# Kernel tuning notes

Measured on AMD Instinct MI355X. Metric: run time of the kernel, lower is better.

The kernel has to match this reference:

```python
import jax, jax.numpy as jnp
import numpy as np

SIGMA = 300.0      # args.sigma (temporal gaussian kernel width, frames)
DECAY = 0.9        # args.memory_decay; avg() uses weight = 1/decay per older entry
W_TIME = 1.0       # args.temporal_weight
ORIG_LOSS = 1.0    # args.originalloss_weight
EPS = 1e-7         # BCE clamp


def _get_msg(bank_values, bank_times, bank_mask, ids, times, future):
    """Vectorized MessagePassing.get_msg: per-(id,time) gather of stored
    messages, temporal-kernel + decay weighted average. Mirrors avg():
    out = sum_i dw_i * kernel_i * v_i / sum_i dw_i, dw_i = (1/decay)^rank_i
    with rank over entries passing the past/future condition, zeros if empty."""
    vals = bank_values[ids]                      # [N, M, C]
    ts = bank_times[ids].astype(jnp.float32)     # [N, M]
    mk = bank_mask[ids]                          # [N, M]
    t0 = times.astype(jnp.float32)[:, None]      # [N, 1]
    cond = (ts > t0) if future else (ts < t0)
    m = (mk & cond).astype(vals.dtype)           # [N, M]
    kern = jnp.exp(-((ts - t0) ** 2) / (2.0 * SIGMA ** 2))
    rank = jnp.cumsum(m, axis=1) - m             # exclusive rank among valid entries
    dw = ((1.0 / DECAY) ** rank) * m             # decay weights, masked
    num = jnp.einsum('nm,nmc->nc', dw * kern, vals)
    den = jnp.sum(dw, axis=1, keepdims=True)     # denominator excludes kernel (as avg())
    msg = jnp.where(den > 0, num / jnp.maximum(den, EPS), 0.0)
    return msg * W_TIME


def _bce(p, t):
    p = jnp.clip(p, EPS, 1.0 - EPS)
    return -jnp.mean(t * jnp.log(p) + (1.0 - t) * jnp.log(1.0 - p))


def setup_inputs() -> dict:
    key = jax.random.key(0)
    k = jax.random.split(key, 8)
    N, C, NUM_IDS, M = 512, 157, 10000, 20
    return {
        'a': jax.random.normal(k[0], (N, C), jnp.float32),
        'aa': jax.random.normal(k[1], (N, C, C), jnp.float32),
        'target': jax.random.uniform(k[2], (N, C), jnp.float32),
        'bank_values': jax.random.uniform(k[3], (NUM_IDS, M, C), jnp.float32),
        'bank_times': jax.random.randint(k[4], (NUM_IDS, M), 0, 1000, jnp.int32),
        'bank_mask': jnp.ones((NUM_IDS, M), dtype=bool),
        'ids': jax.random.randint(k[5], (N,), 0, NUM_IDS, jnp.int32),
        'times': jax.random.randint(k[6], (N,), 0, 1000, jnp.int32),
    }


def reference(a, aa, target, bank_values, bank_times, bank_mask, ids, times):
    # msg/fmsg come from stored (detached) data in the original
    msg = jax.lax.stop_gradient(_get_msg(bank_values, bank_times, bank_mask, ids, times, future=False))
    fmsg = jax.lax.stop_gradient(_get_msg(bank_values, bank_times, bank_mask, ids, times, future=True))
    # qa = a + sum_i aa[n,i,j]*msg[n,i] + sum_j aa[n,i,j]*fmsg[n,j]
    qa = a + jnp.einsum('nij,ni->nj', aa, msg) + jnp.einsum('nij,nj->ni', aa, fmsg)
    qa = jax.nn.sigmoid(qa)
    loss = _bce(qa, target) + _bce(jax.nn.sigmoid(a), target) * ORIG_LOSS
    # training, adjustment=False: pastloss = futureloss = 0
    loss = loss / 3.0
    return qa, loss
```

## Files before the change

### kernel.cpp

```cpp
#include <hip/hip_runtime.h>
#include <math.h>

#define N 512
#define C 157
#define M 20

__device__ __forceinline__ float sigmoidf_(float x) {
    return 1.0f / (1.0f + __expf(-x));
}

__global__ __launch_bounds__(256) void atf_main_kernel(
    const float* __restrict__ a,
    const float* __restrict__ aa,
    const float* __restrict__ target,
    const float* __restrict__ bank_values,
    const int* __restrict__ bank_times,
    const int* __restrict__ bank_mask,
    const int* __restrict__ ids,
    const int* __restrict__ times,
    float* __restrict__ out,
    double* __restrict__ loss_acc)
{
    const int n    = blockIdx.x;
    const int tid  = threadIdx.x;
    const int wave = tid >> 6;
    const int lane = tid & 63;

    __shared__ float s_ts[M];
    __shared__ int   s_mk[M];
    __shared__ float s_msg[C];
    __shared__ float s_fmsg[C];
    __shared__ float s_row[C];
    __shared__ float s_colp[4][C];
    __shared__ float s_red[4];

    const int   id = ids[n];
    const float t0 = (float)times[n];

    if (tid < M) {
        s_ts[tid] = (float)bank_times[(size_t)id * M + tid];
        s_mk[tid] = (bank_mask[(size_t)id * M + tid] != 0) ? 1 : 0;
    }
    __syncthreads();

    if (tid < C) {
        const float inv2s2 = 1.0f / (2.0f * 300.0f * 300.0f);
        const float INVDEC = 1.0f / 0.9f;
        float accP = 0.f, accF = 0.f, denP = 0.f, denF = 0.f;
        float wP = 1.f, wF = 1.f;
        const float* vb = bank_values + (size_t)id * M * C + tid;
        #pragma unroll
        for (int m = 0; m < M; ++m) {
            const float ts = s_ts[m];
            const float d  = ts - t0;
            const float kern = __expf(-d * d * inv2s2);
            const float v = vb[m * C];
            const bool mk = (s_mk[m] != 0);
            if (mk && ts < t0) { accP += wP * kern * v; denP += wP; wP *= INVDEC; }
            if (mk && ts > t0) { accF += wF * kern * v; denF += wF; wF *= INVDEC; }
        }
        s_msg[tid]  = (denP > 0.f) ? accP / fmaxf(denP, 1e-7f) : 0.0f;
        s_fmsg[tid] = (denF > 0.f) ? accF / fmaxf(denF, 1e-7f) : 0.0f;
    }
    __syncthreads();

    const float* aan = aa + (size_t)n * C * C;
    const int j0 = lane, j1 = lane + 64, j2 = lane + 128;
    float col0 = 0.f, col1 = 0.f, col2 = 0.f;
    const float f0 = s_fmsg[j0];
    const float f1 = (j1 < C) ? s_fmsg[j1] : 0.0f;
    const float f2 = (j2 < C) ? s_fmsg[j2] : 0.0f;

    for (int i = wave; i < C; i += 4) {
        const float* row = aan + i * C;
        const float mi = s_msg[i];
        const float v0 = row[j0];
        const float v1 = (j1 < C) ? row[j1] : 0.0f;
        const float v2 = (j2 < C) ? row[j2] : 0.0f;
        col0 += v0 * mi;
        col1 += v1 * mi;
        col2 += v2 * mi;
        float rp = v0 * f0 + v1 * f1 + v2 * f2;
        #pragma unroll
        for (int off = 32; off > 0; off >>= 1) rp += __shfl_down(rp, off, 64);
        if (lane == 0) s_row[i] = rp;
    }
    s_colp[wave][j0] = col0;
    if (j1 < C) s_colp[wave][j1] = col1;
    if (j2 < C) s_colp[wave][j2] = col2;
    __syncthreads();

    float local = 0.0f;
    if (tid < C) {
        const float colsum = s_colp[0][tid] + s_colp[1][tid] + s_colp[2][tid] + s_colp[3][tid];
        const float av = a[(size_t)n * C + tid];
        const float qlin = av + colsum + s_row[tid];
        const float p = sigmoidf_(qlin);
        out[(size_t)n * C + tid] = p;

        const float t = target[(size_t)n * C + tid];
        float pc = fminf(fmaxf(p, 1e-7f), 1.0f - 1e-7f);
        float pa = sigmoidf_(av);
        pa = fminf(fmaxf(pa, 1e-7f), 1.0f - 1e-7f);
        local = t * logf(pc) + (1.0f - t) * logf(1.0f - pc)
              + t * logf(pa) + (1.0f - t) * logf(1.0f - pa);
    }
    #pragma unroll
    for (int off = 32; off > 0; off >>= 1) local += __shfl_down(local, off, 64);
    if (lane == 0) s_red[wave] = local;
    __syncthreads();
    if (tid == 0) {
        const double s = (double)(s_red[0] + s_red[1] + s_red[2] + s_red[3]);
        atomicAdd(loss_acc, s);
    }
}

__global__ void atf_finalize_kernel(const double* __restrict__ loss_acc,
                                    float* __restrict__ out)
{
    out[N * C] = (float)(-(*loss_acc) / ((double)(N * C) * 3.0));
}

extern "C" void kernel_launch(void* const* d_in, const int* in_sizes, int n_in,
                              void* d_out, int out_size, void* d_ws, size_t ws_size,
                              hipStream_t stream) {
    const float* a           = (const float*)d_in[0];
    const float* aa          = (const float*)d_in[1];
    const float* target      = (const float*)d_in[2];
    const float* bank_values = (const float*)d_in[3];
    const int*   bank_times  = (const int*)d_in[4];
    const int*   bank_mask   = (const int*)d_in[5];
    const int*   ids         = (const int*)d_in[6];
    const int*   times       = (const int*)d_in[7];

    float*  out      = (float*)d_out;
    double* loss_acc = (double*)d_ws;

    hipMemsetAsync(d_ws, 0, sizeof(double), stream);
    atf_main_kernel<<<N, 256, 0, stream>>>(a, aa, target, bank_values, bank_times,
                                           bank_mask, ids, times, out, loss_acc);
    atf_finalize_kernel<<<1, 1, 0, stream>>>(loss_acc, out);
}
```

Baseline: 229.7 us.

## Unroll aa row loop by two with nontemporal loads; replace atomic loss with partials

The aa streaming loop now handles two rows per wave per iteration, which puts more independent loads in flight and interleaves two shuffle reductions. The loads use nontemporal hints because aa is read only once. The double atomicAdd and the memset are replaced by per-block float partials that a 256-thread finalize kernel reduces. This removes one launch and the atomic contention, but adds register pressure and a slightly different summation order.

```diff
diff --git a/kernel.cpp b/kernel.cpp
--- a/kernel.cpp
+++ b/kernel.cpp
@@ -7,6 +7,9 @@
 
 __device__ __forceinline__ float sigmoidf_(float x) {
     return 1.0f / (1.0f + __expf(-x));
+}
+__device__ __forceinline__ float ntload(const float* p) {
+    return __builtin_nontemporal_load(p);
 }
 
 __global__ __launch_bounds__(256) void atf_main_kernel(
@@ -19,7 +22,7 @@
     const int* __restrict__ ids,
     const int* __restrict__ times,
     float* __restrict__ out,
-    double* __restrict__ loss_acc)
+    float* __restrict__ loss_part)
 {
     const int n    = blockIdx.x;
     const int tid  = threadIdx.x;
@@ -70,24 +73,44 @@
     const float f0 = s_fmsg[j0];
     const float f1 = (j1 < C) ? s_fmsg[j1] : 0.0f;
     const float f2 = (j2 < C) ? s_fmsg[j2] : 0.0f;
+    const bool ok1 = (j1 < C), ok2 = (j2 < C);
 
-    for (int i = wave; i < C; i += 4) {
-        const float* row = aan + i * C;
-        const float mi = s_msg[i];
-        const float v0 = row[j0];
-        const float v1 = (j1 < C) ? row[j1] : 0.0f;
-        const float v2 = (j2 < C) ? row[j2] : 0.0f;
-        col0 += v0 * mi;
-        col1 += v1 * mi;
-        col2 += v2 * mi;
-        float rp = v0 * f0 + v1 * f1 + v2 * f2;
+    for (int i = wave; i < C; i += 8) {
+        const int ib = i + 4;
+        const float* rowA = aan + i * C;
+        const float mA = s_msg[i];
+        const float a0 = ntload(rowA + j0);
+        const float a1 = ok1 ? ntload(rowA + j1) : 0.0f;
+        const float a2 = ok2 ? ntload(rowA + j2) : 0.0f;
+
+        float b0 = 0.f, b1 = 0.f, b2 = 0.f, mB = 0.f;
+        if (ib < C) {
+            const float* rowB = aan + ib * C;
+            mB = s_msg[ib];
+            b0 = ntload(rowB + j0);
+            b1 = ok1 ? ntload(rowB + j1) : 0.0f;
+            b2 = ok2 ? ntload(rowB + j2) : 0.0f;
+        }
+
+        col0 += a0 * mA + b0 * mB;
+        col1 += a1 * mA + b1 * mB;
+        col2 += a2 * mA + b2 * mB;
+
+        float rpA = a0 * f0 + a1 * f1 + a2 * f2;
+        float rpB = b0 * f0 + b1 * f1 + b2 * f2;
         #pragma unroll
-        for (int off = 32; off > 0; off >>= 1) rp += __shfl_down(rp, off, 64);
-        if (lane == 0) s_row[i] = rp;
+        for (int off = 32; off > 0; off >>= 1) {
+            rpA += __shfl_down(rpA, off, 64);
+            rpB += __shfl_down(rpB, off, 64);
+        }
+        if (lane == 0) {
+            s_row[i] = rpA;
+            if (ib < C) s_row[ib] = rpB;
+        }
     }
     s_colp[wave][j0] = col0;
-    if (j1 < C) s_colp[wave][j1] = col1;
-    if (j2 < C) s_colp[wave][j2] = col2;
+    if (ok1) s_colp[wave][j1] = col1;
+    if (ok2) s_colp[wave][j2] = col2;
     __syncthreads();
 
     float local = 0.0f;
@@ -110,15 +133,28 @@
     if (lane == 0) s_red[wave] = local;
     __syncthreads();
     if (tid == 0) {
-        const double s = (double)(s_red[0] + s_red[1] + s_red[2] + s_red[3]);
-        atomicAdd(loss_acc, s);
+        loss_part[n] = s_red[0] + s_red[1] + s_red[2] + s_red[3];
     }
 }
 
-__global__ void atf_finalize_kernel(const double* __restrict__ loss_acc,
-                                    float* __restrict__ out)
+__global__ __launch_bounds__(256) void atf_finalize_kernel(
+    const float* __restrict__ loss_part,
+    float* __restrict__ out)
 {
-    out[N * C] = (float)(-(*loss_acc) / ((double)(N * C) * 3.0));
+    const int tid  = threadIdx.x;
+    const int wave = tid >> 6;
+    const int lane = tid & 63;
+    __shared__ double s_red[4];
+
+    double local = (double)loss_part[tid] + (double)loss_part[tid + 256];
+    #pragma unroll
+    for (int off = 32; off > 0; off >>= 1) local += __shfl_down(local, off, 64);
+    if (lane == 0) s_red[wave] = local;
+    __syncthreads();
+    if (tid == 0) {
+        const double s = s_red[0] + s_red[1] + s_red[2] + s_red[3];
+        out[N * C] = (float)(-s / ((double)(N * C) * 3.0));
+    }
 }
 
 extern "C" void kernel_launch(void* const* d_in, const int* in_sizes, int n_in,
@@ -133,11 +169,10 @@
     const int*   ids         = (const int*)d_in[6];
     const int*   times       = (const int*)d_in[7];
 
-    float*  out      = (float*)d_out;
-    double* loss_acc = (double*)d_ws;
+    float* out       = (float*)d_out;
+    float* loss_part = (float*)d_ws;
 
-    hipMemsetAsync(d_ws, 0, sizeof(double), stream);
     atf_main_kernel<<<N, 256, 0, stream>>>(a, aa, target, bank_values, bank_times,
-                                           bank_mask, ids, times, out, loss_acc);
-    atf_finalize_kernel<<<1, 1, 0, stream>>>(loss_acc, out);
+                                           bank_mask, ids, times, out, loss_part);
+    atf_finalize_kernel<<<1, 256, 0, stream>>>(loss_part, out);
 }
```

New measurement: 219.0 us. 1.05x faster.

## Split fused kernel into msg, row-split einsum, epilogue and reduction kernels

Applied to the files above, without the earlier changes.

The single per-sample kernel is broken into four launches: message computation, an einsum kernel that splits each sample's 157 rows across 4 blocks (2048 blocks total), an epilogue that sums the partial column results and computes the loss, and a finalize kernel that reduces per-sample loss partials in double instead of using atomics. The aim is more parallelism on the bandwidth-bound aa read (about 50MB) by giving more blocks per CU. In exchange it adds launch overhead and round trips of intermediates through global workspace.

```diff
diff --git a/kernel.cpp b/kernel.cpp
--- a/kernel.cpp
+++ b/kernel.cpp
@@ -9,30 +9,25 @@
     return 1.0f / (1.0f + __expf(-x));
 }
 
-__global__ __launch_bounds__(256) void atf_main_kernel(
-    const float* __restrict__ a,
-    const float* __restrict__ aa,
-    const float* __restrict__ target,
+#define WS_MSG  0
+#define WS_FMSG (N * C)
+#define WS_CP   (2 * N * C)
+#define WS_RS   (6 * N * C)
+#define WS_LP   (7 * N * C)
+
+__global__ __launch_bounds__(256) void atf_msg_kernel(
     const float* __restrict__ bank_values,
     const int* __restrict__ bank_times,
     const int* __restrict__ bank_mask,
     const int* __restrict__ ids,
     const int* __restrict__ times,
-    float* __restrict__ out,
-    double* __restrict__ loss_acc)
+    float* __restrict__ ws)
 {
-    const int n    = blockIdx.x;
-    const int tid  = threadIdx.x;
-    const int wave = tid >> 6;
-    const int lane = tid & 63;
+    const int n   = blockIdx.x;
+    const int tid = threadIdx.x;
 
     __shared__ float s_ts[M];
     __shared__ int   s_mk[M];
-    __shared__ float s_msg[C];
-    __shared__ float s_fmsg[C];
-    __shared__ float s_row[C];
-    __shared__ float s_colp[4][C];
-    __shared__ float s_red[4];
 
     const int   id = ids[n];
     const float t0 = (float)times[n];
@@ -59,42 +54,87 @@
             if (mk && ts < t0) { accP += wP * kern * v; denP += wP; wP *= INVDEC; }
             if (mk && ts > t0) { accF += wF * kern * v; denF += wF; wF *= INVDEC; }
         }
-        s_msg[tid]  = (denP > 0.f) ? accP / fmaxf(denP, 1e-7f) : 0.0f;
-        s_fmsg[tid] = (denF > 0.f) ? accF / fmaxf(denF, 1e-7f) : 0.0f;
+        ws[WS_MSG  + (size_t)n * C + tid] = (denP > 0.f) ? accP / fmaxf(denP, 1e-7f) : 0.0f;
+        ws[WS_FMSG + (size_t)n * C + tid] = (denF > 0.f) ? accF / fmaxf(denF, 1e-7f) : 0.0f;
     }
+}
+
+__global__ __launch_bounds__(256) void atf_einsum_kernel(
+    const float* __restrict__ aa,
+    float* __restrict__ ws)
+{
+    const int n   = blockIdx.x >> 2;
+    const int q   = blockIdx.x & 3;
+    static const int B[5] = {0, 39, 78, 117, 157};
+    const int r0 = B[q], r1 = B[q + 1];
+
+    const int tid  = threadIdx.x;
+    const int wave = tid >> 6;
+    const int lane = tid & 63;
+
+    __shared__ float s_msg[C];
+    __shared__ float s_colp[4][C];
+
+    if (tid < C) s_msg[tid] = ws[WS_MSG + (size_t)n * C + tid];
+
+    const int j0 = lane, j1 = lane + 64, j2 = lane + 128;
+    const bool ok1 = (j1 < C), ok2 = (j2 < C);
+    const float* fm = ws + WS_FMSG + (size_t)n * C;
+    const float f0 = fm[j0];
+    const float f1 = ok1 ? fm[j1] : 0.0f;
+    const float f2 = ok2 ? fm[j2] : 0.0f;
     __syncthreads();
 
     const float* aan = aa + (size_t)n * C * C;
-    const int j0 = lane, j1 = lane + 64, j2 = lane + 128;
-    float col0 = 0.f, col1 = 0.f, col2 = 0.f;
-    const float f0 = s_fmsg[j0];
-    const float f1 = (j1 < C) ? s_fmsg[j1] : 0.0f;
-    const float f2 = (j2 < C) ? s_fmsg[j2] : 0.0f;
+    float* rs = ws + WS_RS + (size_t)n * C;
 
-    for (int i = wave; i < C; i += 4) {
+    float c0 = 0.f, c1 = 0.f, c2 = 0.f;
+    for (int i = r0 + wave; i < r1; i += 4) {
         const float* row = aan + i * C;
+        const float v0 = row[j0];
+        const float v1 = ok1 ? row[j1] : 0.0f;
+        const float v2 = ok2 ? row[j2] : 0.0f;
         const float mi = s_msg[i];
-        const float v0 = row[j0];
-        const float v1 = (j1 < C) ? row[j1] : 0.0f;
-        const float v2 = (j2 < C) ? row[j2] : 0.0f;
-        col0 += v0 * mi;
-        col1 += v1 * mi;
-        col2 += v2 * mi;
+        c0 += v0 * mi;
+        c1 += v1 * mi;
+        c2 += v2 * mi;
         float rp = v0 * f0 + v1 * f1 + v2 * f2;
         #pragma unroll
         for (int off = 32; off > 0; off >>= 1) rp += __shfl_down(rp, off, 64);
-        if (lane == 0) s_row[i] = rp;
+        if (lane == 0) rs[i] = rp;
     }
-    s_colp[wave][j0] = col0;
-    if (j1 < C) s_colp[wave][j1] = col1;
-    if (j2 < C) s_colp[wave][j2] = col2;
+    s_colp[wave][j0] = c0;
+    if (ok1) s_colp[wave][j1] = c1;
+    if (ok2) s_colp[wave][j2] = c2;
     __syncthreads();
+
+    if (tid < C) {
+        ws[WS_CP + ((size_t)(4 * n + q)) * C + tid] =
+            s_colp[0][tid] + s_colp[1][tid] + s_colp[2][tid] + s_colp[3][tid];
+    }
+}
+
+__global__ __launch_bounds__(256) void atf_epilogue_kernel(
+    const float* __restrict__ a,
+    const float* __restrict__ target,
+    float* __restrict__ ws,
+    float* __restrict__ out)
+{
+    const int n    = blockIdx.x;
+    const int tid  = threadIdx.x;
+    const int wave = tid >> 6;
+    const int lane = tid & 63;
+    __shared__ float s_red[4];
 
     float local = 0.0f;
     if (tid < C) {
-        const float colsum = s_colp[0][tid] + s_colp[1][tid] + s_colp[2][tid] + s_colp[3][tid];
+        const float colsum = ws[WS_CP + ((size_t)(4 * n + 0)) * C + tid]
+                           + ws[WS_CP + ((size_t)(4 * n + 1)) * C + tid]
+                           + ws[WS_CP + ((size_t)(4 * n + 2)) * C + tid]
+                           + ws[WS_CP + ((size_t)(4 * n + 3)) * C + tid];
+        const float rowsum = ws[WS_RS + (size_t)n * C + tid];
         const float av = a[(size_t)n * C + tid];
-        const float qlin = av + colsum + s_row[tid];
+        const float qlin = av + colsum + rowsum;
         const float p = sigmoidf_(qlin);
         out[(size_t)n * C + tid] = p;
 
@@ -110,15 +150,28 @@
     if (lane == 0) s_red[wave] = local;
     __syncthreads();
     if (tid == 0) {
-        const double s = (double)(s_red[0] + s_red[1] + s_red[2] + s_red[3]);
-        atomicAdd(loss_acc, s);
+        ws[WS_LP + n] = s_red[0] + s_red[1] + s_red[2] + s_red[3];
     }
 }
 
-__global__ void atf_finalize_kernel(const double* __restrict__ loss_acc,
-                                    float* __restrict__ out)
+__global__ __launch_bounds__(256) void atf_finalize_kernel(
+    const float* __restrict__ loss_part,
+    float* __restrict__ out)
 {
-    out[N * C] = (float)(-(*loss_acc) / ((double)(N * C) * 3.0));
+    const int tid  = threadIdx.x;
+    const int wave = tid >> 6;
+    const int lane = tid & 63;
+    __shared__ double s_red[4];
+
+    double local = (double)loss_part[tid] + (double)loss_part[tid + 256];
+    #pragma unroll
+    for (int off = 32; off > 0; off >>= 1) local += __shfl_down(local, off, 64);
+    if (lane == 0) s_red[wave] = local;
+    __syncthreads();
+    if (tid == 0) {
+        const double s = s_red[0] + s_red[1] + s_red[2] + s_red[3];
+        out[N * C] = (float)(-s / ((double)(N * C) * 3.0));
+    }
 }
 
 extern "C" void kernel_launch(void* const* d_in, const int* in_sizes, int n_in,
@@ -133,11 +186,12 @@
     const int*   ids         = (const int*)d_in[6];
     const int*   times       = (const int*)d_in[7];
 
-    float*  out      = (float*)d_out;
-    double* loss_acc = (double*)d_ws;
+    float* out = (float*)d_out;
+    float* ws  = (float*)d_ws;
 
-    hipMemsetAsync(d_ws, 0, sizeof(double), stream);
-    atf_main_kernel<<<N, 256, 0, stream>>>(a, aa, target, bank_values, bank_times,
-                                           bank_mask, ids, times, out, loss_acc);
-    atf_finalize_kernel<<<1, 1, 0, stream>>>(loss_acc, out);
+    atf_msg_kernel<<<N, 256, 0, stream>>>(bank_values, bank_times, bank_mask,
+                                          ids, times, ws);
+    atf_einsum_kernel<<<N * 4, 256, 0, stream>>>(aa, ws);
+    atf_epilogue_kernel<<<N, 256, 0, stream>>>(a, target, ws, out);
+    atf_finalize_kernel<<<1, 256, 0, stream>>>(ws + WS_LP, out);
 }
```

After: 210.2 us. -8.5%, faster.
